# Optimization experiments

Hardware: AMD Instinct MI355X
Metric: run time of the kernel (lower is better)

## Reference

```python
import jax, jax.numpy as jnp
import numpy as np

THRESH = 0.1          # affinity threshold from init_kwargs
SCALES = (1, 2, 4, 8, 16)  # dyadic diffusion scales 2^0..2^4


def compute_dist(X):
    # X: [N, d] -> squared-euclidean pairwise distances via Gram matrix
    G = X @ X.T
    dg = jnp.diag(G)
    return dg[None, :] + dg[:, None] - 2.0 * G


def _diffuse(P, F):
    # returns [P^1 F, P^2 F, P^4 F, P^8 F, P^16 F] via 16 sequential applies
    outs = []
    cur = F
    for step in range(1, SCALES[-1] + 1):
        cur = P @ cur
        if step in SCALES:
            outs.append(cur)
    return outs


def _wavelet_bank(P, F):
    # lazy diffusion wavelets: psi_0 = I - P, psi_j = P^{2^{j-1}} - P^{2^j}
    lows = [F] + _diffuse(P, F)            # t = 0,1,2,4,8,16
    psis = [lows[j] - lows[j + 1] for j in range(len(lows) - 1)]  # 5 wavelets
    return psis, lows[-1]                  # (wavelet coeffs, low-pass P^16 F)


def _gwt_features(X):
    # X: [N, d] reweighted point cloud -> [N, 16*d] scattering features
    N, d = X.shape
    W = jnp.exp(-compute_dist(X) / 10.0)
    W = jnp.where(W < THRESH, jnp.zeros_like(W), W)   # sparsify affinity
    deg = W.sum(axis=1, keepdims=True)                # self-loop w=1 => deg>=1
    P = 0.5 * (jnp.eye(N, dtype=X.dtype) + W / deg)   # lazy random walk
    psis, low = _wavelet_bank(P, X)
    firsts = [jnp.abs(p) for p in psis]
    U = jnp.concatenate(firsts, axis=1)               # [N, 5*d] diffuse all at once
    psis2, _ = _wavelet_bank(P, U)
    # second order: |psi_{j2} |psi_{j1} x|| only for j2 > j1 (10 pairs)
    seconds = [jnp.abs(psis2[j2][:, : j2 * d]) for j2 in range(1, len(psis2))]
    return jnp.concatenate([low] + firsts + seconds, axis=1)  # [N, (1+5+10)*d]


def setup_inputs() -> dict:
    key = jax.random.key(0)
    k1, k2 = jax.random.split(key)
    point_clouds = jax.random.normal(k1, (4, 2048, 3), dtype=jnp.float32)
    alphas = jax.random.uniform(k2, (4, 3), dtype=jnp.float32)  # learned param
    return {"point_clouds": point_clouds, "alphas": alphas}


def reference(point_clouds, alphas):
    # point_clouds: [B, N, d]; alphas: [K, d]
    Xb = point_clouds[:, None, :, :] * alphas[None, :, None, :]  # [B, K, N, d]
    feats = jax.vmap(jax.vmap(_gwt_features))(Xb)                # [B, K, N, 16d]
    # per-cloud: cat over K along feature dim then mean over nodes == mean then flatten
    return feats.mean(axis=2).reshape(feats.shape[0], -1)        # [B, K*16*d]
```

## Files before the change

### kernel.cpp

```cpp
#include <hip/hip_runtime.h>
#include <hip/hip_bf16.h>


#define NN 2048
#define NPAIR 16

typedef _Float16 half8 __attribute__((ext_vector_type(8)));
typedef _Float16 f16x2 __attribute__((ext_vector_type(2)));
typedef float f32x4 __attribute__((ext_vector_type(4)));

extern "C" __device__ f16x2 __ocml_exp2_2f16(f16x2);

#define C2F 0.28853900817779268f
#define CWF -0.14426950408889634f
#define NL2T 3.3219280948873623f

__global__ __launch_bounds__(256) void initpack_k(const float* __restrict__ pc,
                                                  const float* __restrict__ alphas,
                                                  float* __restrict__ Xs,
                                                  _Float16* __restrict__ XT,
                                                  _Float16* __restrict__ Xp,
                                                  float* __restrict__ outz) {
    int gid = blockIdx.x * 256 + threadIdx.x;
    if (gid >= NPAIR * NN) return;
    if (gid < NPAIR * 48) outz[gid] = 0.f;
    int p = gid >> 11, i = gid & (NN - 1);
    int b = p >> 2, k = p & 3;
    const float* pcr = pc + ((size_t)b * NN + i) * 3;
    const float* al  = alphas + k * 3;
    float x = pcr[0] * al[0], y = pcr[1] * al[1], z = pcr[2] * al[2];
    float q = CWF * (x * x + y * y + z * z);
    float4 o; o.x = x; o.y = y; o.z = z; o.w = q;
    ((float4*)Xs)[gid] = o;
    _Float16* xt = XT + (size_t)p * 16 * NN + i;
    xt[0 * NN] = (_Float16)x;
    xt[1 * NN] = (_Float16)y;
    xt[2 * NN] = (_Float16)z;
    xt[3 * NN] = (_Float16)1.0f;
#pragma unroll
    for (int n = 4; n < 16; ++n) xt[n * NN] = (_Float16)0.f;
    _Float16* xp = Xp + ((size_t)p * 1024 + (i >> 1)) * 8 + (i & 1);
    xp[0] = (_Float16)x; xp[2] = (_Float16)y;
    xp[4] = (_Float16)z; xp[6] = (_Float16)q;
}

template<bool FIRST, bool BUILDU, bool FUSEDRED>
__global__ __launch_bounds__(512, 8)
void apply_k(const float* __restrict__ Xs, const _Float16* __restrict__ Xp,
             float* __restrict__ ihd,
             const _Float16* __restrict__ cur, _Float16* __restrict__ out,
             float* __restrict__ lvl, int t,
             const float* __restrict__ LT1u, const float* __restrict__ LT2r,
             float* __restrict__ fout) {
    __shared__ __align__(16) float smem[8576];
    const int tid  = threadIdx.x;
    const int lane = tid & 63;
    const int wv   = tid >> 6;
    const int p    = blockIdx.y;
    const int m0   = blockIdx.x * 32;
    const int idx16 = lane & 15, quad = lane >> 4;

    {
        const float4* src = (const float4*)(Xp + (size_t)p * 8192);
        float4* dst = (float4*)smem;
        dst[wv * 128 + lane]      = src[wv * 128 + lane];
        dst[wv * 128 + 64 + lane] = src[wv * 128 + 64 + lane];
    }

    f16x2 qi2[2], xx2[2], xy2[2], xz2[2];
#pragma unroll
    for (int s = 0; s < 2; ++s) {
        float4 v = *(const float4*)(Xs + ((size_t)p * NN + m0 + s * 16 + idx16) * 4);
        _Float16 q = (_Float16)(v.w + NL2T);
        _Float16 x = (_Float16)(C2F * v.x);
        _Float16 y = (_Float16)(C2F * v.y);
        _Float16 z = (_Float16)(C2F * v.z);
        qi2[s] = (f16x2){q, q}; xx2[s] = (f16x2){x, x};
        xy2[s] = (f16x2){y, y}; xz2[s] = (f16x2){z, z};
    }
    const f16x2 SC2 = (f16x2){(_Float16)32768.f, (_Float16)32768.f};

    const _Float16* bp = cur + ((size_t)p * 16 + idx16) * NN + wv * 256 + quad * 8;
    f32x4 acc[2] = {{0.f,0.f,0.f,0.f},{0.f,0.f,0.f,0.f}};

    for (int kc = 0; kc < 8; ++kc) {
        const int pb = wv * 128 + kc * 16 + quad * 4;
        half8 bf = *(const half8*)(bp + kc * 32);
        union { f16x2 h2[4]; half8 h8; } af[2];
#pragma unroll
        for (int jp = 0; jp < 4; ++jp) {
            union { float4 f; f16x2 h[4]; } e;
            e.f = ((const float4*)smem)[pb + jp];
#pragma unroll
            for (int s = 0; s < 2; ++s) {
                f16x2 tv = qi2[s] + e.h[3];
                tv = __builtin_elementwise_fma(xx2[s], e.h[0], tv);
                tv = __builtin_elementwise_fma(xy2[s], e.h[1], tv);
                tv = __builtin_elementwise_fma(xz2[s], e.h[2], tv);
                f16x2 u = __builtin_elementwise_min(tv, tv * SC2);
                af[s].h2[jp] = __ocml_exp2_2f16(u);
            }
        }
#pragma unroll
        for (int s = 0; s < 2; ++s)
            acc[s] = __builtin_amdgcn_mfma_f32_16x16x32_f16(af[s].h8, bf, acc[s], 0, 0, 0);
    }

    const int n  = tid >> 5;
    const int rr = tid & 31;
    const int s2 = rr >> 4, mloc = rr & 15;
    const int base = s2 * 256 + (mloc >> 2) * 64 + (mloc & 3);
    const int row = m0 + rr;
    float ihEff;
    if (!FIRST) ihEff = 0.1f * ihd[p * NN + row];

#pragma unroll
    for (int s = 0; s < 2; ++s)
        *(f32x4*)&smem[4096 + wv * 512 + s * 256 + lane * 4] = acc[s];
    __syncthreads();

    float sum = 0.f;
#pragma unroll
    for (int g = 0; g < 8; ++g) sum += smem[4096 + g * 512 + base + n * 4];
    if (FIRST) {
        float deg10 = 0.f;
#pragma unroll
        for (int g = 0; g < 8; ++g) deg10 += smem[4096 + g * 512 + base + 12];
        float ih = 5.0f / deg10;
        if (n == 3) ihd[p * NN + row] = ih;
        ihEff = 0.1f * ih;
    }
    float cv = (float)cur[((size_t)p * 16 + n) * NN + row];
    float o1v = 0.5f * cv + ihEff * sum;
    if (lvl) lvl[(((size_t)p * 5 + t) * 16 + n) * NN + row] = o1v;

    if (FUSEDRED) {
        if (n >= 4) smem[8192 + (n - 4) * 32 + rr] = o1v;
        __syncthreads();
        if (tid < 384) {
            const int f = tid >> 3, g = tid & 7;
            const float* l1 = LT1u + (size_t)p * 5 * 16 * NN;
            const float* l2 = LT2r + (size_t)p * 5 * 16 * NN;
            float s = 0.f;
#pragma unroll
            for (int k = 0; k < 4; ++k) {
                const int m = m0 + g * 4 + k;
                float v;
                if (f < 3) {
                    v = l2[((size_t)3 * 16 + f) * NN + m];
                } else if (f < 18) {
                    int j = (f - 3) / 3, c = (f - 3) % 3;
                    float a = (j == 0) ? Xs[((size_t)p * NN + m) * 4 + c]
                                       : l1[((size_t)(j - 1) * 16 + c) * NN + m];
                    float b = (j < 4) ? l1[((size_t)j * 16 + c) * NN + m]
                                      : l2[((size_t)3 * 16 + c) * NN + m];
                    v = fabsf(a - b);
                } else {
                    int gg = f - 18, j2, uc;
                    if (gg < 3)       { j2 = 1; uc = gg; }
                    else if (gg < 9)  { j2 = 2; uc = gg - 3; }
                    else if (gg < 18) { j2 = 3; uc = gg - 9; }
                    else              { j2 = 4; uc = gg - 18; }
                    float a = l2[((size_t)(j2 - 1) * 16 + uc + 4) * NN + m];
                    float b = (j2 == 4) ? smem[8192 + uc * 32 + (g * 4 + k)]
                                        : l2[((size_t)j2 * 16 + uc + 4) * NN + m];
                    v = fabsf(a - b);
                }
                s += v;
            }
#pragma unroll
            for (int off = 4; off > 0; off >>= 1) s += __shfl_down(s, off, 8);
            if (g == 0) atomicAdd(&fout[p * 48 + f], s * (1.0f / NN));
        }
        return;
    }

    if (!BUILDU) {
        out[((size_t)p * 16 + n) * NN + row] = (_Float16)o1v;
    } else {
        if (n < 3) smem[8192 + n * 32 + rr] = o1v;
        __syncthreads();
        float oval = o1v;
        if (n >= 4) {
            const int u = n - 4, jw = u / 3, c = u - 3 * jw;
            float a = (jw == 0) ? Xs[((size_t)p * NN + row) * 4 + c]
                                : LT1u[(((size_t)p * 5 + (jw - 1)) * 16 + c) * NN + row];
            float bb = (jw == 3) ? smem[8192 + c * 32 + rr]
                                 : LT1u[(((size_t)p * 5 + jw) * 16 + c) * NN + row];
            oval = fabsf(a - bb);
        }
        out[((size_t)p * 16 + n) * NN + row] = (_Float16)oval;
    }
}

extern "C" void kernel_launch(void* const* d_in, const int* in_sizes, int n_in,
                              void* d_out, int out_size, void* d_ws, size_t ws_size,
                              hipStream_t stream) {
    const float* pc     = (const float*)d_in[0];
    const float* alphas = (const float*)d_in[1];
    float* outp = (float*)d_out;

    char* base = (char*)d_ws;
    size_t off = 0;
    auto carve = [&](size_t bytes) -> void* {
        void* r = base + off;
        off = (off + bytes + 255) & ~(size_t)255;
        return r;
    };
    float*     Xs  = (float*)carve((size_t)NPAIR * NN * 4 * sizeof(float));
    _Float16*  Xp  = (_Float16*)carve((size_t)NPAIR * 1024 * 8 * 2);
    float*     ihd = (float*)carve((size_t)NPAIR * NN * sizeof(float));
    _Float16*  XT  = (_Float16*)carve((size_t)NPAIR * 16 * NN * 2);
    _Float16*  pA  = (_Float16*)carve((size_t)NPAIR * 16 * NN * 2);
    _Float16*  pB  = (_Float16*)carve((size_t)NPAIR * 16 * NN * 2);
    float*     LT1 = (float*)carve((size_t)NPAIR * 5 * 16 * NN * sizeof(float));
    float*     LT2 = (float*)carve((size_t)NPAIR * 5 * 16 * NN * sizeof(float));

    dim3 gridA(NN / 32, NPAIR);

    initpack_k<<<dim3((NPAIR * NN) / 256), 256, 0, stream>>>(pc, alphas, Xs, XT, Xp, outp);

    const _Float16* c1 = XT;
    int slot = 0;
    for (int step = 1; step <= 8; ++step) {
        _Float16* o1 = (c1 == pA) ? pB : pA;
        bool sv = (step & (step - 1)) == 0;
        float* lv = sv ? LT1 : nullptr;
        if (step == 1)
            apply_k<true, false, false><<<gridA, 512, 0, stream>>>(Xs, Xp, ihd,
                c1, o1, lv, slot, nullptr, nullptr, nullptr);
        else if (step == 8)
            apply_k<false, true, false><<<gridA, 512, 0, stream>>>(Xs, Xp, ihd,
                c1, o1, lv, slot, LT1, nullptr, nullptr);
        else
            apply_k<false, false, false><<<gridA, 512, 0, stream>>>(Xs, Xp, ihd,
                c1, o1, lv, slot, nullptr, nullptr, nullptr);
        if (sv) ++slot;
        c1 = o1;
    }

    int slot2 = 0;
    for (int i = 1; i <= 16; ++i) {
        _Float16* o1 = (c1 == pA) ? pB : pA;
        bool sv = (i & (i - 1)) == 0;
        if (i == 16) {
            apply_k<false, false, true><<<gridA, 512, 0, stream>>>(Xs, Xp, ihd,
                c1, o1, nullptr, 4, LT1, LT2, outp);
        } else {
            float* lv = sv ? LT2 : nullptr;
            apply_k<false, false, false><<<gridA, 512, 0, stream>>>(Xs, Xp, ihd,
                c1, o1, lv, slot2, nullptr, nullptr, nullptr);
            if (sv) ++slot2;
        }
        c1 = o1;
    }
}
```

Measured before the change: 428.1 us.

## Fuse init into first diffusion step and skip dead feature-column loads and stores

Removes the separate init/pack kernel by computing the scaled coordinates, packed fp16 tiles and the Xs buffer inside the first apply step, which derives its B operand directly from shared memory. Each apply step is specialised by mode so that only the live columns of the 16-wide state (the 3 coordinates in the first pass, the U columns in the late second pass) are loaded and written, and level stores are limited to the columns later consumed. This cuts one launch and some global traffic but adds branching and relies on the exact column-usage bookkeeping across stages.

New measurement: 423.3 us. About the same (-1.1%).

```diff
diff --git a/kernel.cpp b/kernel.cpp
--- a/kernel.cpp
+++ b/kernel.cpp
@@ -15,38 +15,10 @@
 #define CWF -0.14426950408889634f
 #define NL2T 3.3219280948873623f
 
-__global__ __launch_bounds__(256) void initpack_k(const float* __restrict__ pc,
-                                                  const float* __restrict__ alphas,
-                                                  float* __restrict__ Xs,
-                                                  _Float16* __restrict__ XT,
-                                                  _Float16* __restrict__ Xp,
-                                                  float* __restrict__ outz) {
-    int gid = blockIdx.x * 256 + threadIdx.x;
-    if (gid >= NPAIR * NN) return;
-    if (gid < NPAIR * 48) outz[gid] = 0.f;
-    int p = gid >> 11, i = gid & (NN - 1);
-    int b = p >> 2, k = p & 3;
-    const float* pcr = pc + ((size_t)b * NN + i) * 3;
-    const float* al  = alphas + k * 3;
-    float x = pcr[0] * al[0], y = pcr[1] * al[1], z = pcr[2] * al[2];
-    float q = CWF * (x * x + y * y + z * z);
-    float4 o; o.x = x; o.y = y; o.z = z; o.w = q;
-    ((float4*)Xs)[gid] = o;
-    _Float16* xt = XT + (size_t)p * 16 * NN + i;
-    xt[0 * NN] = (_Float16)x;
-    xt[1 * NN] = (_Float16)y;
-    xt[2 * NN] = (_Float16)z;
-    xt[3 * NN] = (_Float16)1.0f;
-#pragma unroll
-    for (int n = 4; n < 16; ++n) xt[n * NN] = (_Float16)0.f;
-    _Float16* xp = Xp + ((size_t)p * 1024 + (i >> 1)) * 8 + (i & 1);
-    xp[0] = (_Float16)x; xp[2] = (_Float16)y;
-    xp[4] = (_Float16)z; xp[6] = (_Float16)q;
-}
-
-template<bool FIRST, bool BUILDU, bool FUSEDRED>
+template<int MODE>
 __global__ __launch_bounds__(512, 8)
-void apply_k(const float* __restrict__ Xs, const _Float16* __restrict__ Xp,
+void apply_k(const float* __restrict__ pc, const float* __restrict__ alphas,
+             float* __restrict__ Xs, _Float16* __restrict__ Xp,
              float* __restrict__ ihd,
              const _Float16* __restrict__ cur, _Float16* __restrict__ out,
              float* __restrict__ lvl, int t,
@@ -59,8 +31,31 @@
     const int p    = blockIdx.y;
     const int m0   = blockIdx.x * 32;
     const int idx16 = lane & 15, quad = lane >> 4;
-
-    {
+    const int b = p >> 2;
+
+    float a0, a1, a2;
+    if (MODE == 0) {
+        const int kk = p & 3;
+        a0 = alphas[kk * 3 + 0]; a1 = alphas[kk * 3 + 1]; a2 = alphas[kk * 3 + 2];
+        if (blockIdx.x == 0 && tid < 48) fout[p * 48 + tid] = 0.f;
+        float4* dst = (float4*)smem;
+#pragma unroll
+        for (int e = 0; e < 2; ++e) {
+            const int idx = wv * 128 + e * 64 + lane;
+            const float* r = pc + ((size_t)b * NN + idx * 2) * 3;
+            float x0 = r[0] * a0, y0 = r[1] * a1, z0 = r[2] * a2;
+            float x1 = r[3] * a0, y1 = r[4] * a1, z1 = r[5] * a2;
+            float q0 = CWF * (x0 * x0 + y0 * y0 + z0 * z0);
+            float q1 = CWF * (x1 * x1 + y1 * y1 + z1 * z1);
+            union { float4 f; f16x2 h[4]; } ev;
+            ev.h[0] = (f16x2){(_Float16)x0, (_Float16)x1};
+            ev.h[1] = (f16x2){(_Float16)y0, (_Float16)y1};
+            ev.h[2] = (f16x2){(_Float16)z0, (_Float16)z1};
+            ev.h[3] = (f16x2){(_Float16)q0, (_Float16)q1};
+            dst[idx] = ev.f;
+            if (blockIdx.x == 0) ((float4*)Xp)[(size_t)p * 1024 + idx] = ev.f;
+        }
+    } else {
         const float4* src = (const float4*)(Xp + (size_t)p * 8192);
         float4* dst = (float4*)smem;
         dst[wv * 128 + lane]      = src[wv * 128 + lane];
@@ -70,27 +65,60 @@
     f16x2 qi2[2], xx2[2], xy2[2], xz2[2];
 #pragma unroll
     for (int s = 0; s < 2; ++s) {
-        float4 v = *(const float4*)(Xs + ((size_t)p * NN + m0 + s * 16 + idx16) * 4);
-        _Float16 q = (_Float16)(v.w + NL2T);
-        _Float16 x = (_Float16)(C2F * v.x);
-        _Float16 y = (_Float16)(C2F * v.y);
-        _Float16 z = (_Float16)(C2F * v.z);
+        const int row = m0 + s * 16 + idx16;
+        float fx, fy, fz, fq;
+        if (MODE == 0) {
+            const float* r = pc + ((size_t)b * NN + row) * 3;
+            fx = r[0] * a0; fy = r[1] * a1; fz = r[2] * a2;
+            fq = CWF * (fx * fx + fy * fy + fz * fz);
+            if (wv == 0 && quad == 0) {
+                float4 o; o.x = fx; o.y = fy; o.z = fz; o.w = fq;
+                *(float4*)(Xs + ((size_t)p * NN + row) * 4) = o;
+            }
+        } else {
+            float4 v = *(const float4*)(Xs + ((size_t)p * NN + row) * 4);
+            fx = v.x; fy = v.y; fz = v.z; fq = v.w;
+        }
+        _Float16 q = (_Float16)(fq + NL2T);
+        _Float16 x = (_Float16)(C2F * fx);
+        _Float16 y = (_Float16)(C2F * fy);
+        _Float16 z = (_Float16)(C2F * fz);
         qi2[s] = (f16x2){q, q}; xx2[s] = (f16x2){x, x};
         xy2[s] = (f16x2){y, y}; xz2[s] = (f16x2){z, z};
     }
     const f16x2 SC2 = (f16x2){(_Float16)32768.f, (_Float16)32768.f};
+    const f16x2 ONE2 = (f16x2){(_Float16)1.f, (_Float16)1.f};
+    const f16x2 ZER2 = (f16x2){(_Float16)0.f, (_Float16)0.f};
 
     const _Float16* bp = cur + ((size_t)p * 16 + idx16) * NN + wv * 256 + quad * 8;
     f32x4 acc[2] = {{0.f,0.f,0.f,0.f},{0.f,0.f,0.f,0.f}};
 
     for (int kc = 0; kc < 8; ++kc) {
         const int pb = wv * 128 + kc * 16 + quad * 4;
-        half8 bf = *(const half8*)(bp + kc * 32);
+        union { f16x2 h2[4]; half8 h8; } bfu;
+        if (MODE != 0) {
+            bool ld;
+            if (MODE == 3)                 ld = true;
+            else if (MODE == 1 || MODE == 2) ld = (idx16 < 3);
+            else if (MODE == 4)            ld = (idx16 >= 3);
+            else                           ld = (idx16 >= 4);
+            if (ld) bfu.h8 = *(const half8*)(bp + kc * 32);
+            else {
+#pragma unroll
+                for (int z = 0; z < 4; ++z) bfu.h2[z] = ZER2;
+            }
+        }
         union { f16x2 h2[4]; half8 h8; } af[2];
 #pragma unroll
         for (int jp = 0; jp < 4; ++jp) {
             union { float4 f; f16x2 h[4]; } e;
             e.f = ((const float4*)smem)[pb + jp];
+            if (MODE == 0) {
+                bfu.h2[jp] = (idx16 == 0) ? e.h[0]
+                           : (idx16 == 1) ? e.h[1]
+                           : (idx16 == 2) ? e.h[2]
+                           : (idx16 == 3) ? ONE2 : ZER2;
+            }
 #pragma unroll
             for (int s = 0; s < 2; ++s) {
                 f16x2 tv = qi2[s] + e.h[3];
@@ -103,7 +131,7 @@
         }
 #pragma unroll
         for (int s = 0; s < 2; ++s)
-            acc[s] = __builtin_amdgcn_mfma_f32_16x16x32_f16(af[s].h8, bf, acc[s], 0, 0, 0);
+            acc[s] = __builtin_amdgcn_mfma_f32_16x16x32_f16(af[s].h8, bfu.h8, acc[s], 0, 0, 0);
     }
 
     const int n  = tid >> 5;
@@ -112,7 +140,7 @@
     const int base = s2 * 256 + (mloc >> 2) * 64 + (mloc & 3);
     const int row = m0 + rr;
     float ihEff;
-    if (!FIRST) ihEff = 0.1f * ihd[p * NN + row];
+    if (MODE != 0) ihEff = 0.1f * ihd[p * NN + row];
 
 #pragma unroll
     for (int s = 0; s < 2; ++s)
@@ -122,7 +150,7 @@
     float sum = 0.f;
 #pragma unroll
     for (int g = 0; g < 8; ++g) sum += smem[4096 + g * 512 + base + n * 4];
-    if (FIRST) {
+    if (MODE == 0) {
         float deg10 = 0.f;
 #pragma unroll
         for (int g = 0; g < 8; ++g) deg10 += smem[4096 + g * 512 + base + 12];
@@ -130,11 +158,46 @@
         if (n == 3) ihd[p * NN + row] = ih;
         ihEff = 0.1f * ih;
     }
-    float cv = (float)cur[((size_t)p * 16 + n) * NN + row];
+    float cv;
+    if (MODE == 0) {
+        cv = (n < 3) ? pc[((size_t)b * NN + row) * 3 + n] * alphas[(p & 3) * 3 + n] : 0.f;
+    } else if (MODE == 1 || MODE == 2) {
+        cv = (n < 3) ? (float)cur[((size_t)p * 16 + n) * NN + row] : 0.f;
+    } else if (MODE == 3) {
+        cv = (float)cur[((size_t)p * 16 + n) * NN + row];
+    } else {
+        cv = (n >= 4) ? (float)cur[((size_t)p * 16 + n) * NN + row] : 0.f;
+    }
     float o1v = 0.5f * cv + ihEff * sum;
-    if (lvl) lvl[(((size_t)p * 5 + t) * 16 + n) * NN + row] = o1v;
-
-    if (FUSEDRED) {
+
+    if (MODE == 0 || MODE == 1) {
+        if (n < 3) {
+            out[((size_t)p * 16 + n) * NN + row] = (_Float16)o1v;
+            if (lvl) lvl[(((size_t)p * 5 + t) * 16 + n) * NN + row] = o1v;
+        }
+    } else if (MODE == 2) {
+        if (n < 3) {
+            lvl[(((size_t)p * 5 + t) * 16 + n) * NN + row] = o1v;
+            smem[8192 + n * 32 + rr] = o1v;
+        }
+        __syncthreads();
+        float oval = o1v;
+        if (n >= 4) {
+            const int u = n - 4, jw = u / 3, c = u - 3 * jw;
+            float a = (jw == 0) ? Xs[((size_t)p * NN + row) * 4 + c]
+                                : LT1u[(((size_t)p * 5 + (jw - 1)) * 16 + c) * NN + row];
+            float bb = (jw == 3) ? smem[8192 + c * 32 + rr]
+                                 : LT1u[(((size_t)p * 5 + jw) * 16 + c) * NN + row];
+            oval = fabsf(a - bb);
+        }
+        out[((size_t)p * 16 + n) * NN + row] = (_Float16)oval;
+    } else if (MODE == 3) {
+        out[((size_t)p * 16 + n) * NN + row] = (_Float16)o1v;
+        if (lvl && (n >= 4 || (t == 3 && n < 3)))
+            lvl[(((size_t)p * 5 + t) * 16 + n) * NN + row] = o1v;
+    } else if (MODE == 4) {
+        if (n >= 4) out[((size_t)p * 16 + n) * NN + row] = (_Float16)o1v;
+    } else {
         if (n >= 4) smem[8192 + (n - 4) * 32 + rr] = o1v;
         __syncthreads();
         if (tid < 384) {
@@ -152,9 +215,9 @@
                     int j = (f - 3) / 3, c = (f - 3) % 3;
                     float a = (j == 0) ? Xs[((size_t)p * NN + m) * 4 + c]
                                        : l1[((size_t)(j - 1) * 16 + c) * NN + m];
-                    float b = (j < 4) ? l1[((size_t)j * 16 + c) * NN + m]
-                                      : l2[((size_t)3 * 16 + c) * NN + m];
-                    v = fabsf(a - b);
+                    float bb = (j < 4) ? l1[((size_t)j * 16 + c) * NN + m]
+                                       : l2[((size_t)3 * 16 + c) * NN + m];
+                    v = fabsf(a - bb);
                 } else {
                     int gg = f - 18, j2, uc;
                     if (gg < 3)       { j2 = 1; uc = gg; }
@@ -162,9 +225,9 @@
                     else if (gg < 18) { j2 = 3; uc = gg - 9; }
                     else              { j2 = 4; uc = gg - 18; }
                     float a = l2[((size_t)(j2 - 1) * 16 + uc + 4) * NN + m];
-                    float b = (j2 == 4) ? smem[8192 + uc * 32 + (g * 4 + k)]
-                                        : l2[((size_t)j2 * 16 + uc + 4) * NN + m];
-                    v = fabsf(a - b);
+                    float bb = (j2 == 4) ? smem[8192 + uc * 32 + (g * 4 + k)]
+                                         : l2[((size_t)j2 * 16 + uc + 4) * NN + m];
+                    v = fabsf(a - bb);
                 }
                 s += v;
             }
@@ -172,24 +235,6 @@
             for (int off = 4; off > 0; off >>= 1) s += __shfl_down(s, off, 8);
             if (g == 0) atomicAdd(&fout[p * 48 + f], s * (1.0f / NN));
         }
-        return;
-    }
-
-    if (!BUILDU) {
-        out[((size_t)p * 16 + n) * NN + row] = (_Float16)o1v;
-    } else {
-        if (n < 3) smem[8192 + n * 32 + rr] = o1v;
-        __syncthreads();
-        float oval = o1v;
-        if (n >= 4) {
-            const int u = n - 4, jw = u / 3, c = u - 3 * jw;
-            float a = (jw == 0) ? Xs[((size_t)p * NN + row) * 4 + c]
-                                : LT1u[(((size_t)p * 5 + (jw - 1)) * 16 + c) * NN + row];
-            float bb = (jw == 3) ? smem[8192 + c * 32 + rr]
-                                 : LT1u[(((size_t)p * 5 + jw) * 16 + c) * NN + row];
-            oval = fabsf(a - bb);
-        }
-        out[((size_t)p * 16 + n) * NN + row] = (_Float16)oval;
     }
 }
 
@@ -210,7 +255,6 @@
     float*     Xs  = (float*)carve((size_t)NPAIR * NN * 4 * sizeof(float));
     _Float16*  Xp  = (_Float16*)carve((size_t)NPAIR * 1024 * 8 * 2);
     float*     ihd = (float*)carve((size_t)NPAIR * NN * sizeof(float));
-    _Float16*  XT  = (_Float16*)carve((size_t)NPAIR * 16 * NN * 2);
     _Float16*  pA  = (_Float16*)carve((size_t)NPAIR * 16 * NN * 2);
     _Float16*  pB  = (_Float16*)carve((size_t)NPAIR * 16 * NN * 2);
     float*     LT1 = (float*)carve((size_t)NPAIR * 5 * 16 * NN * sizeof(float));
@@ -218,23 +262,20 @@
 
     dim3 gridA(NN / 32, NPAIR);
 
-    initpack_k<<<dim3((NPAIR * NN) / 256), 256, 0, stream>>>(pc, alphas, Xs, XT, Xp, outp);
-
-    const _Float16* c1 = XT;
-    int slot = 0;
-    for (int step = 1; step <= 8; ++step) {
+    apply_k<0><<<gridA, 512, 0, stream>>>(pc, alphas, Xs, Xp, ihd,
+        nullptr, pA, LT1, 0, nullptr, nullptr, outp);
+    const _Float16* c1 = pA;
+    int slot = 1;
+
+    for (int step = 2; step <= 8; ++step) {
         _Float16* o1 = (c1 == pA) ? pB : pA;
         bool sv = (step & (step - 1)) == 0;
-        float* lv = sv ? LT1 : nullptr;
-        if (step == 1)
-            apply_k<true, false, false><<<gridA, 512, 0, stream>>>(Xs, Xp, ihd,
-                c1, o1, lv, slot, nullptr, nullptr, nullptr);
-        else if (step == 8)
-            apply_k<false, true, false><<<gridA, 512, 0, stream>>>(Xs, Xp, ihd,
-                c1, o1, lv, slot, LT1, nullptr, nullptr);
+        if (step == 8)
+            apply_k<2><<<gridA, 512, 0, stream>>>(pc, alphas, Xs, Xp, ihd,
+                c1, o1, LT1, 3, LT1, nullptr, nullptr);
         else
-            apply_k<false, false, false><<<gridA, 512, 0, stream>>>(Xs, Xp, ihd,
-                c1, o1, lv, slot, nullptr, nullptr, nullptr);
+            apply_k<1><<<gridA, 512, 0, stream>>>(pc, alphas, Xs, Xp, ihd,
+                c1, o1, sv ? LT1 : nullptr, slot, nullptr, nullptr, nullptr);
         if (sv) ++slot;
         c1 = o1;
     }
@@ -242,15 +283,17 @@
     int slot2 = 0;
     for (int i = 1; i <= 16; ++i) {
         _Float16* o1 = (c1 == pA) ? pB : pA;
-        bool sv = (i & (i - 1)) == 0;
         if (i == 16) {
-            apply_k<false, false, true><<<gridA, 512, 0, stream>>>(Xs, Xp, ihd,
+            apply_k<5><<<gridA, 512, 0, stream>>>(pc, alphas, Xs, Xp, ihd,
                 c1, o1, nullptr, 4, LT1, LT2, outp);
+        } else if (i <= 8) {
+            bool sv = (i & (i - 1)) == 0;
+            apply_k<3><<<gridA, 512, 0, stream>>>(pc, alphas, Xs, Xp, ihd,
+                c1, o1, sv ? LT2 : nullptr, slot2, nullptr, nullptr, nullptr);
+            if (sv) ++slot2;
         } else {
-            float* lv = sv ? LT2 : nullptr;
-            apply_k<false, false, false><<<gridA, 512, 0, stream>>>(Xs, Xp, ihd,
-                c1, o1, lv, slot2, nullptr, nullptr, nullptr);
-            if (sv) ++slot2;
+            apply_k<4><<<gridA, 512, 0, stream>>>(pc, alphas, Xs, Xp, ihd,
+                c1, o1, nullptr, 0, nullptr, nullptr, nullptr);
         }
         c1 = o1;
     }
```
